# Kernel tuning notes

Hardware: AMD Instinct MI355X
Metric: run time of the kernel (lower is better)

Reference implementation:

```python
import jax, jax.numpy as jnp
import numpy as np

STRIDES = (8, 16, 32)
FEAT_SIZES = ((80, 80), (40, 40), (20, 20))  # (h, w) per level for 640x640 input
OFFSET = 0.5
NMS_K = 300
IOU_THR = 0.65
EPS = 1e-7


def make_priors():
    """MlvlPointGenerator.grid_priors with with_stride=True, flattened over levels."""
    pts, strs = [], []
    for (h, w), s in zip(FEAT_SIZES, STRIDES):
        xs = (jnp.arange(w, dtype=jnp.float32) + OFFSET) * s
        ys = (jnp.arange(h, dtype=jnp.float32) + OFFSET) * s
        yy, xx = jnp.meshgrid(ys, xs, indexing='ij')
        pts.append(jnp.stack([xx.reshape(-1), yy.reshape(-1)], -1))
        strs.append(jnp.full((h * w, 2), float(s), dtype=jnp.float32))
    return jnp.concatenate(pts, 0), jnp.concatenate(strs, 0)  # [N,2], [N,2]


def pairwise_iou(boxes):  # boxes [K,4] xyxy
    area = jnp.clip(boxes[:, 2] - boxes[:, 0], 0) * jnp.clip(boxes[:, 3] - boxes[:, 1], 0)
    lt = jnp.maximum(boxes[:, None, :2], boxes[None, :, :2])
    rb = jnp.minimum(boxes[:, None, 2:], boxes[None, :, 2:])
    wh = jnp.clip(rb - lt, 0)
    inter = wh[..., 0] * wh[..., 1]
    union = area[:, None] + area[None, :] - inter
    return inter / (union + EPS)


def nms_keep(boxes):  # boxes [K,4] sorted by descending score -> bool keep mask [K]
    K = boxes.shape[0]
    iou = pairwise_iou(boxes)
    idx = jnp.arange(K)

    def body(i, keep):
        sup = (iou[i] > IOU_THR) & (idx > i) & keep[i]
        return keep & ~sup

    return jax.lax.fori_loop(0, K, body, jnp.ones((K,), dtype=bool))


def setup_inputs() -> dict:
    key = jax.random.key(0)
    k1, k2, k3, k4, k5 = jax.random.split(key, 5)
    B, N, K = 128, 8400, 17
    return {
        'cls_scores': jax.random.normal(k1, (B, N, 1), jnp.float32),
        'bbox_preds': jax.random.normal(k2, (B, N, 4), jnp.float32),
        'objectness': jax.random.normal(k3, (B, N), jnp.float32),
        'kpt_offsets': jax.random.normal(k4, (B, N, K, 2), jnp.float32),
        'kpt_vis_preds': jax.random.normal(k5, (B, N, K), jnp.float32),
    }


def reference(cls_scores, bbox_preds, objectness, kpt_offsets, kpt_vis_preds):
    priors, strides = make_priors()  # [N,2] each
    # bbox decode: center-offset + exp wh, YOLOX style
    xy = bbox_preds[..., :2] * strides + priors            # [B,N,2]
    wh = jnp.exp(bbox_preds[..., 2:4]) * strides           # [B,N,2]
    boxes = jnp.concatenate([xy - wh * 0.5, xy + wh * 0.5], -1)  # [B,N,4]
    scores = jax.nn.sigmoid(cls_scores[..., 0]) * jax.nn.sigmoid(objectness)  # [B,N]
    # keypoint decode
    kpts = kpt_offsets * strides[:, None, :] + priors[:, None, :]  # [B,N,K,2]
    B, N, K, _ = kpts.shape
    kpts_flat = kpts.reshape(B, N, K * 2)
    vis = jax.nn.sigmoid(kpt_vis_preds)                    # [B,N,K]
    # fixed-size top-k pre-NMS selection
    top_vals, top_idx = jax.lax.top_k(scores, NMS_K)       # [B,NMS_K]
    gather = lambda x: jnp.take_along_axis(x, top_idx[..., None], axis=1)
    boxes_k = gather(boxes)       # [B,NMS_K,4]
    kpts_k = gather(kpts_flat)    # [B,NMS_K,2K]
    vis_k = gather(vis)           # [B,NMS_K,K]
    keep = jax.vmap(nms_keep)(boxes_k)                      # [B,NMS_K] bool
    final_scores = top_vals * keep.astype(top_vals.dtype)
    # [B, NMS_K, 4 + 1 + 2K + K]
    return jnp.concatenate([boxes_k, final_scores[..., None], kpts_k, vis_k], -1)
```

## Files before the change

kernel.cpp:

```cpp
#include <hip/hip_runtime.h>
#include <math.h>

#define BATCH 128
#define NANCH 8400
#define NMSK  300
#define KPT   17
#define OUTC  56
#define CAND  768
#define NTHR  1024

__device__ __forceinline__ void prior_of(int i, float& stride, float& cx, float& cy) {
    int row, col;
    if (i < 6400)      { stride = 8.0f;  row = i / 80;              col = i - row * 80; }
    else if (i < 8000) { int ii = i - 6400; stride = 16.0f; row = ii / 40; col = ii - row * 40; }
    else               { int ii = i - 8000; stride = 32.0f; row = ii / 20; col = ii - row * 20; }
    cx = ((float)col + 0.5f) * stride;
    cy = ((float)row + 0.5f) * stride;
}

__global__ __launch_bounds__(NTHR) void fused_kernel(
    const float* __restrict__ cls, const float* __restrict__ obj,
    const float* __restrict__ bbox, const float* __restrict__ kofs,
    const float* __restrict__ kvis, float* __restrict__ out)
{
    const int b = blockIdx.x;
    const int tid = threadIdx.x;
    const int lane = tid & 63;

    __shared__ __align__(16) unsigned int sc[NANCH];
    __shared__ unsigned int hist[256];
    __shared__ unsigned int suf[256];
    __shared__ unsigned int sh_prefix, sh_k, sh_cnt;
    __shared__ unsigned long long ckey[CAND];
    __shared__ float bx1[NMSK], by1[NMSK], bx2[NMSK], by2[NMSK], area[NMSK];
    __shared__ float sval[NMSK], pst[NMSK], ppx[NMSK], ppy[NMSK];
    __shared__ int   sidx[NMSK];
    __shared__ unsigned long long supl[NMSK * 6];
    __shared__ unsigned long long keepw[5];

    {
        const float4* c4 = (const float4*)(cls + (size_t)b * NANCH);
        const float4* o4 = (const float4*)(obj + (size_t)b * NANCH);
        for (int i = tid; i < NANCH / 4; i += NTHR) {
            float4 cv = c4[i];
            float4 ov = o4[i];
            float sa0 = 1.0f / (1.0f + (float)exp(-(double)cv.x));
            float sa1 = 1.0f / (1.0f + (float)exp(-(double)cv.y));
            float sa2 = 1.0f / (1.0f + (float)exp(-(double)cv.z));
            float sa3 = 1.0f / (1.0f + (float)exp(-(double)cv.w));
            float so0 = 1.0f / (1.0f + (float)exp(-(double)ov.x));
            float so1 = 1.0f / (1.0f + (float)exp(-(double)ov.y));
            float so2 = 1.0f / (1.0f + (float)exp(-(double)ov.z));
            float so3 = 1.0f / (1.0f + (float)exp(-(double)ov.w));
            sc[4 * i + 0] = __float_as_uint(sa0 * so0);
            sc[4 * i + 1] = __float_as_uint(sa1 * so1);
            sc[4 * i + 2] = __float_as_uint(sa2 * so2);
            sc[4 * i + 3] = __float_as_uint(sa3 * so3);
        }
    }
    if (tid == 0) { sh_prefix = 0u; sh_k = NMSK; sh_cnt = 0u; }
    __syncthreads();

    for (int r = 3; r >= 0; --r) {
        if (tid < 256) hist[tid] = 0u;
        __syncthreads();
        unsigned int pfx  = sh_prefix;
        unsigned int kcur = sh_k;
        for (int base = 0; base < NANCH; base += NTHR) {
            int i = base + tid;
            bool valid = (i < NANCH);
            unsigned int key = valid ? sc[i] : 0u;
            bool match = valid && ((r == 3) || ((key >> ((r + 1) * 8)) == pfx));
            unsigned int bin = (key >> (r * 8)) & 0xFFu;
            unsigned long long todo = __ballot(match);
            while (todo) {
                int leader = (int)__ffsll((long long)todo) - 1;
                unsigned int lb = (unsigned int)__shfl((int)bin, leader, 64);
                unsigned long long peers = __ballot(match && (bin == lb)) & todo;
                if (lane == leader)
                    atomicAdd(&hist[lb], (unsigned int)__popcll(peers));
                todo &= ~peers;
            }
        }
        __syncthreads();
        if (tid < 64) {
            int l = tid;
            unsigned int b0 = hist[4 * l + 0], b1 = hist[4 * l + 1];
            unsigned int b2 = hist[4 * l + 2], b3 = hist[4 * l + 3];
            unsigned int tot = b0 + b1 + b2 + b3;
            unsigned int v = tot;
            #pragma unroll
            for (int d = 1; d < 64; d <<= 1) {
                unsigned int t2 = (unsigned int)__shfl_down((int)v, d, 64);
                if (l + d < 64) v += t2;
            }
            unsigned int above = v - tot;
            suf[4 * l + 3] = above + b3;
            suf[4 * l + 2] = above + b3 + b2;
            suf[4 * l + 1] = above + b3 + b2 + b1;
            suf[4 * l + 0] = above + tot;
        }
        __syncthreads();
        if (tid < 256) {
            unsigned int ge     = suf[tid];
            unsigned int genext = (tid < 255) ? suf[tid + 1] : 0u;
            if (ge >= kcur && genext < kcur) {
                sh_prefix = (pfx << 8) | (unsigned int)tid;
                sh_k      = kcur - genext;
            }
        }
        __syncthreads();
    }

    unsigned int pivot_bits = sh_prefix;
    for (int base = 0; base < NANCH; base += NTHR) {
        int i = base + tid;
        bool valid = (i < NANCH);
        unsigned int key = valid ? sc[i] : 0u;
        bool pred = valid && (key >= pivot_bits);
        unsigned long long m = __ballot(pred);
        unsigned int cnt = (unsigned int)__popcll(m);
        unsigned int wbase = 0u;
        if (lane == 0 && cnt) wbase = atomicAdd(&sh_cnt, cnt);
        wbase = (unsigned int)__shfl((int)wbase, 0, 64);
        if (pred) {
            unsigned int p = wbase + (unsigned int)__popcll(m & ((1ull << lane) - 1ull));
            if (p < CAND)
                ckey[p] = ((unsigned long long)key << 32)
                        | (unsigned long long)(0xFFFFFFFFu - (unsigned int)i);
        }
    }
    __syncthreads();
    unsigned int M = sh_cnt; if (M > CAND) M = CAND;

    if (tid < (int)M) {
        unsigned long long mine = ckey[tid];
        int rank = 0;
        for (unsigned int t2 = 0; t2 < M; ++t2) rank += (ckey[t2] > mine) ? 1 : 0;
        if (rank < NMSK) {
            sidx[rank] = (int)(0xFFFFFFFFu - (unsigned int)(mine & 0xFFFFFFFFull));
            sval[rank] = __uint_as_float((unsigned int)(mine >> 32));
        }
    }
    __syncthreads();

    if (tid < NMSK) {
        int j = tid;
        int i = sidx[j];
        float stride, cx, cy;
        prior_of(i, stride, cx, cy);
        pst[j] = stride; ppx[j] = cx; ppy[j] = cy;
        float4 bb = *(const float4*)(bbox + ((size_t)b * NANCH + (size_t)i) * 4);
        float x = bb.x * stride + cx;
        float y = bb.y * stride + cy;
        float w = expf(bb.z) * stride;
        float h = expf(bb.w) * stride;
        float x1 = x - 0.5f * w, y1 = y - 0.5f * h;
        float x2 = x + 0.5f * w, y2 = y + 0.5f * h;
        bx1[j] = x1; by1[j] = y1; bx2[j] = x2; by2[j] = y2;
        area[j] = fmaxf(x2 - x1, 0.0f) * fmaxf(y2 - y1, 0.0f);
    }
    __syncthreads();

    for (int t = tid; t < NMSK * 5; t += NTHR) {
        int w = t / NMSK;
        int i = t - w * NMSK;
        int jlo = w * 64; if (jlo < i + 1) jlo = i + 1;
        int jhi = w * 64 + 64; if (jhi > NMSK) jhi = NMSK;
        unsigned long long m = 0;
        float ax1 = bx1[i], ay1 = by1[i], ax2 = bx2[i], ay2 = by2[i], aa = area[i];
        for (int j = jlo; j < jhi; ++j) {
            float lx = fmaxf(ax1, bx1[j]);
            float ly = fmaxf(ay1, by1[j]);
            float rx = fminf(ax2, bx2[j]);
            float ry = fminf(ay2, by2[j]);
            float iw = fmaxf(rx - lx, 0.0f);
            float ih = fmaxf(ry - ly, 0.0f);
            float inter = iw * ih;
            float iou = inter / (aa + area[j] - inter + 1e-7f);
            if (iou > 0.65f) m |= 1ull << (j & 63);
        }
        supl[i * 6 + w] = m;
    }
    __syncthreads();

    if (tid < 64) {
        unsigned long long k0 = ~0ull, k1 = ~0ull, k2 = ~0ull, k3 = ~0ull;
        unsigned long long k4 = (1ull << (NMSK - 256)) - 1ull;
        const unsigned long long* sp = supl;
        #define GSTEP(KW, I) \
            if (((KW) >> ((I) & 63)) & 1ull) { \
                const unsigned long long* s = sp + (size_t)(I) * 6; \
                k0 &= ~s[0]; k1 &= ~s[1]; k2 &= ~s[2]; k3 &= ~s[3]; k4 &= ~s[4]; }
        for (int i = 0;   i < 64;   ++i) { GSTEP(k0, i) }
        for (int i = 64;  i < 128;  ++i) { GSTEP(k1, i) }
        for (int i = 128; i < 192;  ++i) { GSTEP(k2, i) }
        for (int i = 192; i < 256;  ++i) { GSTEP(k3, i) }
        for (int i = 256; i < NMSK; ++i) { GSTEP(k4, i) }
        #undef GSTEP
        if (tid == 0) { keepw[0] = k0; keepw[1] = k1; keepw[2] = k2; keepw[3] = k3; keepw[4] = k4; }
    } else {
        const float* kof = kofs + (size_t)b * NANCH * 34;
        const float* kvi = kvis + (size_t)b * NANCH * KPT;
        float* ob = out + (size_t)b * NMSK * OUTC;
        for (int e = tid - 64; e < NMSK * 51; e += NTHR - 64) {
            int j  = e / 51;
            int ci = e - j * 51;
            int i  = sidx[j];
            float v;
            if (ci < 34) {
                float off = kof[(size_t)i * 34 + ci];
                v = off * pst[j] + ((ci & 1) ? ppy[j] : ppx[j]);
            } else {
                float x = kvi[(size_t)i * KPT + (ci - 34)];
                v = 1.0f / (1.0f + expf(-x));
            }
            ob[j * OUTC + 5 + ci] = v;
        }
    }
    __syncthreads();

    float* ob = out + (size_t)b * NMSK * OUTC;
    for (int t = tid; t < NMSK * 5; t += NTHR) {
        int j  = t / 5;
        int ci = t - j * 5;
        float v;
        if (ci == 0)      v = bx1[j];
        else if (ci == 1) v = by1[j];
        else if (ci == 2) v = bx2[j];
        else if (ci == 3) v = by2[j];
        else {
            bool kp = (keepw[j >> 6] >> (j & 63)) & 1ull;
            v = kp ? sval[j] : 0.0f;
        }
        ob[j * OUTC + ci] = v;
    }
}

extern "C" void kernel_launch(void* const* d_in, const int* in_sizes, int n_in,
                              void* d_out, int out_size, void* d_ws, size_t ws_size,
                              hipStream_t stream) {
    const float* cls  = (const float*)d_in[0];
    const float* bbox = (const float*)d_in[1];
    const float* obj  = (const float*)d_in[2];
    const float* kofs = (const float*)d_in[3];
    const float* kvis = (const float*)d_in[4];
    float* out = (float*)d_out;

    (void)d_ws; (void)ws_size;

    fused_kernel<<<BATCH, NTHR, 0, stream>>>(cls, obj, bbox, kofs, kvis, out);
}
```

Baseline: 286.9 us.

## Split fused kernel into scores, select and keypoint kernels with single-pass histogram

The single per-batch kernel becomes three launches. A grid-wide scores kernel computes sigmoid products into workspace. A select kernel does top-k with one 8192-bin histogram pass instead of four 8-bit radix passes, and runs NMS using register-resident suppression rows broadcast with readlane. A keypoint gather kernel uses two blocks per batch. The aim is to use more CUs than the 128 single blocks did and to cut barrier-heavy radix rounds. The costs are extra launches and global round-trips for scores and indices, plus reliance on the candidate buffer (raised to 1024) holding every entry in the pivot bin.

```diff
diff --git a/kernel.cpp b/kernel.cpp
--- a/kernel.cpp
+++ b/kernel.cpp
@@ -6,8 +6,10 @@
 #define NMSK  300
 #define KPT   17
 #define OUTC  56
-#define CAND  768
+#define CAND  1024
 #define NTHR  1024
+#define NBIN  8192
+#define BSHIFT 19
 
 __device__ __forceinline__ void prior_of(int i, float& stride, float& cx, float& cy) {
     int row, col;
@@ -18,101 +20,107 @@
     cy = ((float)row + 0.5f) * stride;
 }
 
-__global__ __launch_bounds__(NTHR) void fused_kernel(
+__global__ __launch_bounds__(256) void scores_kernel(
     const float* __restrict__ cls, const float* __restrict__ obj,
-    const float* __restrict__ bbox, const float* __restrict__ kofs,
-    const float* __restrict__ kvis, float* __restrict__ out)
+    unsigned int* __restrict__ sc)
+{
+    int i = blockIdx.x * 256 + threadIdx.x;
+    float4 cv = ((const float4*)cls)[i];
+    float4 ov = ((const float4*)obj)[i];
+    float sa0 = 1.0f / (1.0f + (float)exp(-(double)cv.x));
+    float sa1 = 1.0f / (1.0f + (float)exp(-(double)cv.y));
+    float sa2 = 1.0f / (1.0f + (float)exp(-(double)cv.z));
+    float sa3 = 1.0f / (1.0f + (float)exp(-(double)cv.w));
+    float so0 = 1.0f / (1.0f + (float)exp(-(double)ov.x));
+    float so1 = 1.0f / (1.0f + (float)exp(-(double)ov.y));
+    float so2 = 1.0f / (1.0f + (float)exp(-(double)ov.z));
+    float so3 = 1.0f / (1.0f + (float)exp(-(double)ov.w));
+    uint4 r;
+    r.x = __float_as_uint(sa0 * so0);
+    r.y = __float_as_uint(sa1 * so1);
+    r.z = __float_as_uint(sa2 * so2);
+    r.w = __float_as_uint(sa3 * so3);
+    ((uint4*)sc)[i] = r;
+}
+
+__global__ __launch_bounds__(NTHR) void select_kernel(
+    const unsigned int* __restrict__ sc_g, const float* __restrict__ bbox,
+    float* __restrict__ out, int* __restrict__ sidx_g)
 {
     const int b = blockIdx.x;
     const int tid = threadIdx.x;
     const int lane = tid & 63;
+    const int wv = tid >> 6;
 
     __shared__ __align__(16) unsigned int sc[NANCH];
-    __shared__ unsigned int hist[256];
-    __shared__ unsigned int suf[256];
-    __shared__ unsigned int sh_prefix, sh_k, sh_cnt;
+    __shared__ __align__(16) unsigned int hist[NBIN];
+    __shared__ unsigned int wtot[16], wab[16];
+    __shared__ unsigned int sh_pivot, sh_cnt;
     __shared__ unsigned long long ckey[CAND];
     __shared__ float bx1[NMSK], by1[NMSK], bx2[NMSK], by2[NMSK], area[NMSK];
-    __shared__ float sval[NMSK], pst[NMSK], ppx[NMSK], ppy[NMSK];
+    __shared__ float sval[NMSK];
     __shared__ int   sidx[NMSK];
     __shared__ unsigned long long supl[NMSK * 6];
     __shared__ unsigned long long keepw[5];
 
     {
-        const float4* c4 = (const float4*)(cls + (size_t)b * NANCH);
-        const float4* o4 = (const float4*)(obj + (size_t)b * NANCH);
-        for (int i = tid; i < NANCH / 4; i += NTHR) {
-            float4 cv = c4[i];
-            float4 ov = o4[i];
-            float sa0 = 1.0f / (1.0f + (float)exp(-(double)cv.x));
-            float sa1 = 1.0f / (1.0f + (float)exp(-(double)cv.y));
-            float sa2 = 1.0f / (1.0f + (float)exp(-(double)cv.z));
-            float sa3 = 1.0f / (1.0f + (float)exp(-(double)cv.w));
-            float so0 = 1.0f / (1.0f + (float)exp(-(double)ov.x));
-            float so1 = 1.0f / (1.0f + (float)exp(-(double)ov.y));
-            float so2 = 1.0f / (1.0f + (float)exp(-(double)ov.z));
-            float so3 = 1.0f / (1.0f + (float)exp(-(double)ov.w));
-            sc[4 * i + 0] = __float_as_uint(sa0 * so0);
-            sc[4 * i + 1] = __float_as_uint(sa1 * so1);
-            sc[4 * i + 2] = __float_as_uint(sa2 * so2);
-            sc[4 * i + 3] = __float_as_uint(sa3 * so3);
-        }
-    }
-    if (tid == 0) { sh_prefix = 0u; sh_k = NMSK; sh_cnt = 0u; }
-    __syncthreads();
-
-    for (int r = 3; r >= 0; --r) {
-        if (tid < 256) hist[tid] = 0u;
-        __syncthreads();
-        unsigned int pfx  = sh_prefix;
-        unsigned int kcur = sh_k;
-        for (int base = 0; base < NANCH; base += NTHR) {
-            int i = base + tid;
-            bool valid = (i < NANCH);
-            unsigned int key = valid ? sc[i] : 0u;
-            bool match = valid && ((r == 3) || ((key >> ((r + 1) * 8)) == pfx));
-            unsigned int bin = (key >> (r * 8)) & 0xFFu;
-            unsigned long long todo = __ballot(match);
-            while (todo) {
-                int leader = (int)__ffsll((long long)todo) - 1;
-                unsigned int lb = (unsigned int)__shfl((int)bin, leader, 64);
-                unsigned long long peers = __ballot(match && (bin == lb)) & todo;
-                if (lane == leader)
-                    atomicAdd(&hist[lb], (unsigned int)__popcll(peers));
-                todo &= ~peers;
-            }
-        }
-        __syncthreads();
-        if (tid < 64) {
-            int l = tid;
-            unsigned int b0 = hist[4 * l + 0], b1 = hist[4 * l + 1];
-            unsigned int b2 = hist[4 * l + 2], b3 = hist[4 * l + 3];
-            unsigned int tot = b0 + b1 + b2 + b3;
-            unsigned int v = tot;
-            #pragma unroll
-            for (int d = 1; d < 64; d <<= 1) {
-                unsigned int t2 = (unsigned int)__shfl_down((int)v, d, 64);
-                if (l + d < 64) v += t2;
-            }
-            unsigned int above = v - tot;
-            suf[4 * l + 3] = above + b3;
-            suf[4 * l + 2] = above + b3 + b2;
-            suf[4 * l + 1] = above + b3 + b2 + b1;
-            suf[4 * l + 0] = above + tot;
-        }
-        __syncthreads();
-        if (tid < 256) {
-            unsigned int ge     = suf[tid];
-            unsigned int genext = (tid < 255) ? suf[tid + 1] : 0u;
-            if (ge >= kcur && genext < kcur) {
-                sh_prefix = (pfx << 8) | (unsigned int)tid;
-                sh_k      = kcur - genext;
-            }
-        }
-        __syncthreads();
-    }
-
-    unsigned int pivot_bits = sh_prefix;
+        const uint4* s4 = (const uint4*)(sc_g + (size_t)b * NANCH);
+        uint4* d4 = (uint4*)sc;
+        for (int i = tid; i < NANCH / 4; i += NTHR) d4[i] = s4[i];
+        uint4 z; z.x = z.y = z.z = z.w = 0u;
+        uint4* h4 = (uint4*)hist;
+        for (int i = tid; i < NBIN / 4; i += NTHR) h4[i] = z;
+        if (tid == 0) sh_cnt = 0u;
+    }
+    __syncthreads();
+
+    for (int i = tid; i < NANCH; i += NTHR) atomicAdd(&hist[sc[i] >> BSHIFT], 1u);
+    __syncthreads();
+
+    unsigned int s7[8];
+    {
+        uint4 a = ((uint4*)hist)[2 * tid];
+        uint4 c = ((uint4*)hist)[2 * tid + 1];
+        unsigned int h0 = a.x, h1 = a.y, h2 = a.z, h3 = a.w;
+        unsigned int h4 = c.x, h5 = c.y, h6 = c.z, h7 = c.w;
+        s7[7] = h7;
+        s7[6] = s7[7] + h6; s7[5] = s7[6] + h5; s7[4] = s7[5] + h4;
+        s7[3] = s7[4] + h3; s7[2] = s7[3] + h2; s7[1] = s7[2] + h1;
+        s7[0] = s7[1] + h0;
+    }
+    unsigned int T = s7[0];
+    unsigned int v = T;
+    #pragma unroll
+    for (int d = 1; d < 64; d <<= 1) {
+        unsigned int t2 = (unsigned int)__shfl_down((int)v, d, 64);
+        if (lane + d < 64) v += t2;
+    }
+    unsigned int aiw = v - T;
+    if (lane == 0) wtot[wv] = v;
+    __syncthreads();
+    if (tid < 16) {
+        unsigned int wa = 0;
+        for (int q = tid + 1; q < 16; ++q) wa += wtot[q];
+        wab[tid] = wa;
+    }
+    __syncthreads();
+    {
+        unsigned int ag = wab[wv] + aiw;
+        #pragma unroll
+        for (int k = 0; k < 8; ++k) hist[8 * tid + k] = ag + s7[k];
+    }
+    __syncthreads();
+
+    #pragma unroll
+    for (int k = 0; k < 8; ++k) {
+        unsigned int bin = 8 * (unsigned)tid + k;
+        unsigned int ge = hist[bin];
+        unsigned int gn = (bin < NBIN - 1) ? hist[bin + 1] : 0u;
+        if (ge >= NMSK && gn < NMSK) sh_pivot = bin;
+    }
+    __syncthreads();
+    unsigned int pivot_bits = sh_pivot << BSHIFT;
+
     for (int base = 0; base < NANCH; base += NTHR) {
         int i = base + tid;
         bool valid = (i < NANCH);
@@ -149,7 +157,6 @@
         int i = sidx[j];
         float stride, cx, cy;
         prior_of(i, stride, cx, cy);
-        pst[j] = stride; ppx[j] = cx; ppy[j] = cy;
         float4 bb = *(const float4*)(bbox + ((size_t)b * NANCH + (size_t)i) * 4);
         float x = bb.x * stride + cx;
         float y = bb.y * stride + cy;
@@ -185,55 +192,83 @@
     __syncthreads();
 
     if (tid < 64) {
-        unsigned long long k0 = ~0ull, k1 = ~0ull, k2 = ~0ull, k3 = ~0ull;
-        unsigned long long k4 = (1ull << (NMSK - 256)) - 1ull;
-        const unsigned long long* sp = supl;
-        #define GSTEP(KW, I) \
-            if (((KW) >> ((I) & 63)) & 1ull) { \
-                const unsigned long long* s = sp + (size_t)(I) * 6; \
-                k0 &= ~s[0]; k1 &= ~s[1]; k2 &= ~s[2]; k3 &= ~s[3]; k4 &= ~s[4]; }
-        for (int i = 0;   i < 64;   ++i) { GSTEP(k0, i) }
-        for (int i = 64;  i < 128;  ++i) { GSTEP(k1, i) }
-        for (int i = 128; i < 192;  ++i) { GSTEP(k2, i) }
-        for (int i = 192; i < 256;  ++i) { GSTEP(k3, i) }
-        for (int i = 256; i < NMSK; ++i) { GSTEP(k4, i) }
-        #undef GSTEP
-        if (tid == 0) { keepw[0] = k0; keepw[1] = k1; keepw[2] = k2; keepw[3] = k3; keepw[4] = k4; }
+        int j = tid;
+        unsigned long long keep0 = ~0ull, keep1 = ~0ull, keep2 = ~0ull, keep3 = ~0ull;
+        unsigned long long keep4 = (1ull << (NMSK - 256)) - 1ull;
+        #define CHUNK(C, KC, IMAX) { \
+            int r = (C) * 64 + j; \
+            unsigned int lo0=0,hi0=0,lo1=0,hi1=0,lo2=0,hi2=0,lo3=0,hi3=0,lo4=0,hi4=0; \
+            if (r < NMSK) { \
+                unsigned long long w0 = supl[r*6+0], w1 = supl[r*6+1], w2 = supl[r*6+2]; \
+                unsigned long long w3 = supl[r*6+3], w4 = supl[r*6+4]; \
+                lo0=(unsigned int)w0; hi0=(unsigned int)(w0>>32); \
+                lo1=(unsigned int)w1; hi1=(unsigned int)(w1>>32); \
+                lo2=(unsigned int)w2; hi2=(unsigned int)(w2>>32); \
+                lo3=(unsigned int)w3; hi3=(unsigned int)(w3>>32); \
+                lo4=(unsigned int)w4; hi4=(unsigned int)(w4>>32); } \
+            for (int bi = 0; bi < (IMAX); ++bi) { \
+                if ((KC >> bi) & 1ull) { \
+                    unsigned long long s0 = ((unsigned long long)__builtin_amdgcn_readlane(hi0,bi)<<32) | __builtin_amdgcn_readlane(lo0,bi); \
+                    unsigned long long s1 = ((unsigned long long)__builtin_amdgcn_readlane(hi1,bi)<<32) | __builtin_amdgcn_readlane(lo1,bi); \
+                    unsigned long long s2 = ((unsigned long long)__builtin_amdgcn_readlane(hi2,bi)<<32) | __builtin_amdgcn_readlane(lo2,bi); \
+                    unsigned long long s3 = ((unsigned long long)__builtin_amdgcn_readlane(hi3,bi)<<32) | __builtin_amdgcn_readlane(lo3,bi); \
+                    unsigned long long s4 = ((unsigned long long)__builtin_amdgcn_readlane(hi4,bi)<<32) | __builtin_amdgcn_readlane(lo4,bi); \
+                    keep0 &= ~s0; keep1 &= ~s1; keep2 &= ~s2; keep3 &= ~s3; keep4 &= ~s4; } } }
+        CHUNK(0, keep0, 64)
+        CHUNK(1, keep1, 64)
+        CHUNK(2, keep2, 64)
+        CHUNK(3, keep3, 64)
+        CHUNK(4, keep4, NMSK - 256)
+        #undef CHUNK
+        if (j == 0) { keepw[0]=keep0; keepw[1]=keep1; keepw[2]=keep2; keepw[3]=keep3; keepw[4]=keep4; }
     } else {
-        const float* kof = kofs + (size_t)b * NANCH * 34;
-        const float* kvi = kvis + (size_t)b * NANCH * KPT;
+        int* sg = sidx_g + (size_t)b * NMSK;
         float* ob = out + (size_t)b * NMSK * OUTC;
-        for (int e = tid - 64; e < NMSK * 51; e += NTHR - 64) {
-            int j  = e / 51;
-            int ci = e - j * 51;
-            int i  = sidx[j];
-            float v;
-            if (ci < 34) {
-                float off = kof[(size_t)i * 34 + ci];
-                v = off * pst[j] + ((ci & 1) ? ppy[j] : ppx[j]);
-            } else {
-                float x = kvi[(size_t)i * KPT + (ci - 34)];
-                v = 1.0f / (1.0f + expf(-x));
-            }
-            ob[j * OUTC + 5 + ci] = v;
-        }
-    }
-    __syncthreads();
-
+        for (int t = tid - 64; t < NMSK; t += NTHR - 64) sg[t] = sidx[t];
+        for (int t = tid - 64; t < NMSK * 4; t += NTHR - 64) {
+            int j = t >> 2, ci = t & 3;
+            float vv = (ci == 0) ? bx1[j] : (ci == 1) ? by1[j] : (ci == 2) ? bx2[j] : by2[j];
+            ob[j * OUTC + ci] = vv;
+        }
+    }
+    __syncthreads();
+
+    if (tid < NMSK) {
+        bool kp = (keepw[tid >> 6] >> (tid & 63)) & 1ull;
+        out[(size_t)b * NMSK * OUTC + (size_t)tid * OUTC + 4] = kp ? sval[tid] : 0.0f;
+    }
+}
+
+__global__ __launch_bounds__(512) void kpt_kernel(
+    const int* __restrict__ sidx_g, const float* __restrict__ kofs,
+    const float* __restrict__ kvis, float* __restrict__ out)
+{
+    const int b = blockIdx.x >> 1;
+    const int h = blockIdx.x & 1;
+    const int tid = threadIdx.x;
+    __shared__ int si[NMSK];
+    if (tid < NMSK) si[tid] = sidx_g[(size_t)b * NMSK + tid];
+    __syncthreads();
+    const float* kof = kofs + (size_t)b * NANCH * 34;
+    const float* kvi = kvis + (size_t)b * NANCH * KPT;
     float* ob = out + (size_t)b * NMSK * OUTC;
-    for (int t = tid; t < NMSK * 5; t += NTHR) {
-        int j  = t / 5;
-        int ci = t - j * 5;
+    const int half = (NMSK * 51) / 2;
+    const int e0 = h * half;
+    for (int e = e0 + tid; e < e0 + half; e += 512) {
+        int j  = e / 51;
+        int ci = e - j * 51;
+        int i  = si[j];
+        float stride, cx, cy;
+        prior_of(i, stride, cx, cy);
         float v;
-        if (ci == 0)      v = bx1[j];
-        else if (ci == 1) v = by1[j];
-        else if (ci == 2) v = bx2[j];
-        else if (ci == 3) v = by2[j];
-        else {
-            bool kp = (keepw[j >> 6] >> (j & 63)) & 1ull;
-            v = kp ? sval[j] : 0.0f;
-        }
-        ob[j * OUTC + ci] = v;
+        if (ci < 34) {
+            float off = kof[(size_t)i * 34 + ci];
+            v = off * stride + ((ci & 1) ? cy : cx);
+        } else {
+            float x = kvi[(size_t)i * KPT + (ci - 34)];
+            v = 1.0f / (1.0f + expf(-x));
+        }
+        ob[j * OUTC + 5 + ci] = v;
     }
 }
 
@@ -247,7 +282,10 @@
     const float* kvis = (const float*)d_in[4];
     float* out = (float*)d_out;
 
-    (void)d_ws; (void)ws_size;
-
-    fused_kernel<<<BATCH, NTHR, 0, stream>>>(cls, obj, bbox, kofs, kvis, out);
-}
+    unsigned int* sc = (unsigned int*)d_ws;
+    int* sidx_g = (int*)((char*)d_ws + (size_t)BATCH * NANCH * sizeof(unsigned int));
+
+    scores_kernel<<<(BATCH * NANCH / 4) / 256, 256, 0, stream>>>(cls, obj, sc);
+    select_kernel<<<BATCH, NTHR, 0, stream>>>(sc, bbox, out, sidx_g);
+    kpt_kernel<<<BATCH * 2, 512, 0, stream>>>(sidx_g, kofs, kvis, out);
+}
```

After: 325.7 us. +13.5%, slower.
